# Performance work log

Measured on AMD Instinct MI355X. Metric: run time of the kernel, lower is better.

## Reference

```python
import jax, jax.numpy as jnp
import numpy as np

N_CLASSES = 19


def setup_inputs() -> dict:
    key = jax.random.key(0)
    k1, k2 = jax.random.split(key)
    embedding = jax.random.normal(k1, (4, 32, 128, 128), dtype=jnp.float32)
    label = jax.random.randint(k2, (4, 512, 512), 0, N_CLASSES, dtype=jnp.int64)
    return {"embedding": embedding, "label": label}


def _discriminative_loss(embedding, label, n_classes=N_CLASSES):
    N, H, W = label.shape
    C = embedding.shape[1]
    # bilinear upsample embedding to label resolution (F.upsample mode='bilinear')
    emb = jax.image.resize(embedding, (N, C, H, W), method="bilinear")
    HW = H * W
    emb = emb.reshape(N, C, HW).transpose(0, 2, 1)          # (N, HW, C)
    lab = label.reshape(N, HW)                               # (N, HW)

    onehot = jax.nn.one_hot(lab, n_classes, dtype=emb.dtype)  # (N, HW, K)
    count = onehot.sum(1)                                    # (N, K)
    mask = (count > 0).astype(emb.dtype)                     # (N, K)

    # per-class embedding sum and (biased, /(count+1)) mean
    cls_sum = jnp.einsum("npc,npk->nkc", emb, onehot)       # (N, K, C)
    cls_mean = cls_sum / (count[:, :, None] + 1.0)           # (N, K, C)

    # intra-class: per-pixel squared distance to own-class mean, mean over C
    mean_pp = jnp.take_along_axis(cls_mean, lab[:, :, None], axis=1)  # (N, HW, C)
    d2 = jnp.mean((emb - mean_pp) ** 2, axis=-1)             # (N, HW)
    intra_per_cls = jnp.einsum("np,npk->nk", d2, onehot) / (count + 1.0)  # (N, K)
    n_fg = mask[:, 1:].sum(1)                                # (N,)
    l2_intra = (intra_per_cls[:, 1:] * mask[:, 1:]).sum(1) / n_fg  # (N,)

    # inter-class: pairwise mean squared distance between class means
    diff = cls_mean[:, :, None, :] - cls_mean[:, None, :, :]  # (N, K, K, C)
    inter = jnp.mean(diff ** 2, axis=-1)                     # (N, K, K)
    inter = inter * mask[:, None, :] * mask[:, :, None]
    l2_inter = inter[:, 1:, 1:].reshape(N, -1).sum(1) / (n_fg * n_fg)  # (N,)

    return l2_intra - l2_inter


def reference(embedding, label):
    return _discriminative_loss(embedding, label)
```

## Files before the change

### kernel.cpp

```cpp
#include <hip/hip_runtime.h>

#define NIMG 4
#define NCLS 19
#define CCH  32
#define LH   128
#define LW   128
#define HH   512
#define WW   512
#define HWQ  (LH*LW)
#define HWP  (HH*WW)

#define TR 8
#define TC 16
#define NTX (LW/TC)
#define NTY (LH/TR)
#define NTILE (NTY*NTX)
#define TCELLS (TR*TC)
#define HALO_R (TR*4+4)
#define HALO_C (TC*4+4)

#define QB 64

__device__ __forceinline__ void taps(int v, int lim, int& i0, int& i1, float& f) {
    int r = v & 3;
    int b = (v >> 2) + ((r < 2) ? -1 : 0);
    f = 0.125f + 0.25f * (float)((r + 2) & 3);
    i0 = b < 0 ? 0 : b;
    i1 = (b + 1 > lim) ? lim : (b + 1);
}

__global__ __launch_bounds__(256) void k_field(const float* __restrict__ E,
        const int* __restrict__ lab, float* __restrict__ P_sum, float* __restrict__ P_cnt) {
    int tile = blockIdx.x, n = blockIdx.y;
    int ty = tile >> 3, tx = tile & 7;
    int Y0 = ty * TR, X0 = tx * TC;
    __shared__ float A[TCELLS * NCLS];
    __shared__ float red[8 * NCLS * CCH];
    int tid = threadIdx.x;
    for (int i = tid; i < TCELLS * NCLS; i += 256) A[i] = 0.f;
    __syncthreads();

    const int* ln = lab + (size_t)n * HWP;
    int h_lo = Y0 * 4 - 2, w_lo = X0 * 4 - 2;
    for (int i = tid; i < HALO_R * HALO_C; i += 256) {
        int hr = i / HALO_C, wc = i - hr * HALO_C;
        int h = h_lo + hr, w = w_lo + wc;
        if (h < 0 || h >= HH || w < 0 || w >= WW) continue;
        int L = ln[h * WW + w];
        int y0, y1, x0, x1; float fy, fx;
        taps(h, LH - 1, y0, y1, fy);
        taps(w, LW - 1, x0, x1, fx);
        int yy[2] = {y0, y1}; float wy[2] = {1.f - fy, fy};
        int xx[2] = {x0, x1}; float wx[2] = {1.f - fx, fx};
#pragma unroll
        for (int a = 0; a < 2; a++) {
#pragma unroll
            for (int b = 0; b < 2; b++) {
                int ry = yy[a] - Y0, rx = xx[b] - X0;
                if (ry >= 0 && ry < TR && rx >= 0 && rx < TC)
                    atomicAdd(&A[(ry * TC + rx) * NCLS + L], wy[a] * wx[b]);
            }
        }
    }
    __syncthreads();

    int g = tid >> 5, c = tid & 31;
    const float* Ec = E + ((size_t)n * CCH + c) * HWQ;
    float acc[NCLS];
#pragma unroll
    for (int k = 0; k < NCLS; k++) acc[k] = 0.f;
#pragma unroll
    for (int j = 0; j < TCELLS / 8; j++) {
        int cell = g * (TCELLS / 8) + j;
        int cy = cell >> 4, cx = cell & 15;
        float e = Ec[(Y0 + cy) * LW + (X0 + cx)];
        const float* Ar = &A[cell * NCLS];
#pragma unroll
        for (int k = 0; k < NCLS; k++) acc[k] = fmaf(Ar[k], e, acc[k]);
    }
#pragma unroll
    for (int k = 0; k < NCLS; k++) red[(g * NCLS + k) * CCH + c] = acc[k];
    __syncthreads();

    float* Ps = P_sum + (size_t)(n * NTILE + tile) * (NCLS * CCH);
    for (int idx = tid; idx < NCLS * CCH; idx += 256) {
        float s = 0.f;
#pragma unroll
        for (int gg = 0; gg < 8; gg++) s += red[gg * NCLS * CCH + idx];
        Ps[idx] = s;
    }
    if (tid < NCLS) {
        float s = 0.f;
        for (int cell = 0; cell < TCELLS; cell++) s += A[cell * NCLS + tid];
        P_cnt[(size_t)(n * NTILE + tile) * NCLS + tid] = s;
    }
}

__global__ __launch_bounds__(256) void k_quad(const float* __restrict__ E,
        const int* __restrict__ lab, float* __restrict__ P_S2) {
    int n = blockIdx.y;
    int q = blockIdx.x * 256 + threadIdx.x;
    int by = q >> 7, bx = q & 127;
    __shared__ float accS2[NCLS];
    if (threadIdx.x < NCLS) accS2[threadIdx.x] = 0.f;
    __syncthreads();

    const float* En = E + (size_t)n * CCH * HWQ;
    int r0 = (by == 0) ? 0 : by - 1;
    int r2 = (by == LH - 1) ? LH - 1 : by + 1;
    int c0 = (bx == 0) ? 0 : bx - 1;
    int c2 = (bx == LW - 1) ? LW - 1 : bx + 1;
    int o0 = r0 * LW, o1 = by * LW, o2 = r2 * LW;

    float d2[16];
#pragma unroll
    for (int i = 0; i < 16; i++) d2[i] = 0.f;

    for (int c = 0; c < CCH; c++) {
        const float* Ep = En + (size_t)c * HWQ;
        float e00 = Ep[o0 + c0], e01 = Ep[o0 + bx], e02 = Ep[o0 + c2];
        float e10 = Ep[o1 + c0], e11 = Ep[o1 + bx], e12 = Ep[o1 + c2];
        float e20 = Ep[o2 + c0], e21 = Ep[o2 + bx], e22 = Ep[o2 + c2];
        float dy0 = e10 - e00, dy1 = e11 - e01, dy2 = e12 - e02;
        float dz0 = e20 - e10, dz1 = e21 - e11, dz2 = e22 - e12;
        float ry[4][3];
        ry[0][0] = fmaf(0.625f, dy0, e00); ry[0][1] = fmaf(0.625f, dy1, e01); ry[0][2] = fmaf(0.625f, dy2, e02);
        ry[1][0] = fmaf(0.875f, dy0, e00); ry[1][1] = fmaf(0.875f, dy1, e01); ry[1][2] = fmaf(0.875f, dy2, e02);
        ry[2][0] = fmaf(0.125f, dz0, e10); ry[2][1] = fmaf(0.125f, dz1, e11); ry[2][2] = fmaf(0.125f, dz2, e12);
        ry[3][0] = fmaf(0.375f, dz0, e10); ry[3][1] = fmaf(0.375f, dz1, e11); ry[3][2] = fmaf(0.375f, dz2, e12);
#pragma unroll
        for (int r = 0; r < 4; r++) {
            float da = ry[r][1] - ry[r][0], db = ry[r][2] - ry[r][1];
            float v0 = fmaf(0.625f, da, ry[r][0]);
            float v1 = fmaf(0.875f, da, ry[r][0]);
            float v2 = fmaf(0.125f, db, ry[r][1]);
            float v3 = fmaf(0.375f, db, ry[r][1]);
            d2[r * 4 + 0] = fmaf(v0, v0, d2[r * 4 + 0]);
            d2[r * 4 + 1] = fmaf(v1, v1, d2[r * 4 + 1]);
            d2[r * 4 + 2] = fmaf(v2, v2, d2[r * 4 + 2]);
            d2[r * 4 + 3] = fmaf(v3, v3, d2[r * 4 + 3]);
        }
    }
    const int* lp = lab + (size_t)n * HWP + (by * 4) * WW + bx * 4;
#pragma unroll
    for (int r = 0; r < 4; r++) {
        int4 l4 = *(const int4*)(lp + r * WW);
        atomicAdd(&accS2[l4.x], d2[r * 4 + 0]);
        atomicAdd(&accS2[l4.y], d2[r * 4 + 1]);
        atomicAdd(&accS2[l4.z], d2[r * 4 + 2]);
        atomicAdd(&accS2[l4.w], d2[r * 4 + 3]);
    }
    __syncthreads();
    if (threadIdx.x < NCLS)
        P_S2[(size_t)(n * QB + blockIdx.x) * NCLS + threadIdx.x] = accS2[threadIdx.x];
}

__global__ __launch_bounds__(384) void k_final(const float* __restrict__ P_sum,
        const float* __restrict__ P_cnt, const float* __restrict__ P_S2,
        float* __restrict__ out) {
    int n = blockIdx.x, t = threadIdx.x;
    __shared__ float csum[NCLS * 33];
    __shared__ float m[NCLS * 33];
    __shared__ float cnt[NCLS];
    __shared__ float S2[NCLS];
    __shared__ float sIntra, sNfg, sInter;

    if (t == 0) sInter = 0.f;
    if (t < NCLS) {
        float s = 0.f;
        const float* p = P_cnt + (size_t)n * NTILE * NCLS + t;
        for (int b = 0; b < NTILE; b++) s += p[b * NCLS];
        cnt[t] = s;
        float s2 = 0.f;
        const float* p2 = P_S2 + (size_t)n * QB * NCLS + t;
        for (int b = 0; b < QB; b++) s2 += p2[b * NCLS];
        S2[t] = s2;
    }
    for (int idx = t; idx < NCLS * CCH; idx += 384) {
        float s = 0.f;
        const float* p = P_sum + (size_t)n * NTILE * NCLS * CCH + idx;
        for (int b = 0; b < NTILE; b++) s += p[b * NCLS * CCH];
        csum[(idx >> 5) * 33 + (idx & 31)] = s;
    }
    __syncthreads();
    for (int idx = t; idx < NCLS * CCH; idx += 384) {
        int k = idx >> 5, c = idx & 31;
        m[k * 33 + c] = csum[k * 33 + c] / (cnt[k] + 1.f);
    }
    __syncthreads();

    float vi = 0.f, fg = 0.f;
    if (t >= 1 && t < NCLS && cnt[t] > 0.f) {
        fg = 1.f;
        float dot = 0.f, mm = 0.f;
        for (int c = 0; c < CCH; c++) {
            float mv = m[t * 33 + c];
            dot = fmaf(mv, csum[t * 33 + c], dot);
            mm = fmaf(mv, mv, mm);
        }
        vi = (S2[t] - 2.f * dot + cnt[t] * mm) * (1.f / 32.f) / (cnt[t] + 1.f);
    }
#pragma unroll
    for (int s_ = 32; s_ >= 1; s_ >>= 1) { vi += __shfl_xor(vi, s_); fg += __shfl_xor(fg, s_); }
    if (t == 0) { sIntra = vi; sNfg = fg; }

    float ve = 0.f;
    if (t < 324) {
        int j = 1 + t / 18, k = 1 + t % 18;
        if (cnt[j] > 0.f && cnt[k] > 0.f) {
            float s = 0.f;
            for (int c = 0; c < CCH; c++) {
                float d = m[j * 33 + c] - m[k * 33 + c];
                s = fmaf(d, d, s);
            }
            ve = s * (1.f / 32.f);
        }
    }
#pragma unroll
    for (int s_ = 32; s_ >= 1; s_ >>= 1) ve += __shfl_xor(ve, s_);
    if ((t & 63) == 0) atomicAdd(&sInter, ve);
    __syncthreads();
    if (t == 0) out[n] = sIntra / sNfg - sInter / (sNfg * sNfg);
}

extern "C" void kernel_launch(void* const* d_in, const int* in_sizes, int n_in,
                              void* d_out, int out_size, void* d_ws, size_t ws_size,
                              hipStream_t stream) {
    const float* E = (const float*)d_in[0];
    const int* lab = (const int*)d_in[1];
    float* out = (float*)d_out;

    float* ws = (float*)d_ws;
    float* P_sum = ws;
    float* P_cnt = P_sum + (size_t)NIMG * NTILE * NCLS * CCH;
    float* P_S2  = P_cnt + (size_t)NIMG * NTILE * NCLS;

    k_field<<<dim3(NTILE, NIMG), dim3(256), 0, stream>>>(E, lab, P_sum, P_cnt);
    k_quad <<<dim3(QB, NIMG),    dim3(256), 0, stream>>>(E, lab, P_S2);
    k_final<<<dim3(NIMG),        dim3(384), 0, stream>>>(P_sum, P_cnt, P_S2, out);
}
```

Measured before the change: 119.6 us.

## Merge field and quad kernels into one launch with LDS-staged embedding tiles

The per-tile class-sum kernel and the per-pixel squared-norm kernel are fused into one launch whose blocks branch on blockIdx, removing a kernel launch and letting both workloads run concurrently. The field path now stages the embedding tile in padded LDS and reduces across half-waves with shuffles, cutting strided global reads. The quad path splits channels across two halves of each block, so it launches twice as many blocks over rows. The partial buffers are transposed so the final kernel can reduce counts and S2 with coalesced loads and wave shuffles. In exchange, the split quad path issues more label loads and LDS atomics, and blocks with different LDS and register needs share one kernel, which may limit occupancy.

Result: no change. 120.1 us (+0.4%).

```diff
diff --git a/kernel.cpp b/kernel.cpp
--- a/kernel.cpp
+++ b/kernel.cpp
@@ -12,14 +12,16 @@
 
 #define TR 8
 #define TC 16
-#define NTX (LW/TC)
-#define NTY (LH/TR)
-#define NTILE (NTY*NTX)
-#define TCELLS (TR*TC)
-#define HALO_R (TR*4+4)
-#define HALO_C (TC*4+4)
-
-#define QB 64
+#define NTILE 128
+#define TCELLS 128
+#define HALO_R 36
+#define HALO_C 68
+#define QROWS 128
+
+#define L_ET  0
+#define L_A   4224
+#define L_RED 6656
+#define LDS_FLOATS 9088
 
 __device__ __forceinline__ void taps(int v, int lim, int& i0, int& i1, float& f) {
     int r = v & 3;
@@ -29,162 +31,175 @@
     i1 = (b + 1 > lim) ? lim : (b + 1);
 }
 
-__global__ __launch_bounds__(256) void k_field(const float* __restrict__ E,
-        const int* __restrict__ lab, float* __restrict__ P_sum, float* __restrict__ P_cnt) {
-    int tile = blockIdx.x, n = blockIdx.y;
-    int ty = tile >> 3, tx = tile & 7;
-    int Y0 = ty * TR, X0 = tx * TC;
-    __shared__ float A[TCELLS * NCLS];
-    __shared__ float red[8 * NCLS * CCH];
-    int tid = threadIdx.x;
-    for (int i = tid; i < TCELLS * NCLS; i += 256) A[i] = 0.f;
-    __syncthreads();
-
-    const int* ln = lab + (size_t)n * HWP;
-    int h_lo = Y0 * 4 - 2, w_lo = X0 * 4 - 2;
-    for (int i = tid; i < HALO_R * HALO_C; i += 256) {
-        int hr = i / HALO_C, wc = i - hr * HALO_C;
-        int h = h_lo + hr, w = w_lo + wc;
-        if (h < 0 || h >= HH || w < 0 || w >= WW) continue;
-        int L = ln[h * WW + w];
-        int y0, y1, x0, x1; float fy, fx;
-        taps(h, LH - 1, y0, y1, fy);
-        taps(w, LW - 1, x0, x1, fx);
-        int yy[2] = {y0, y1}; float wy[2] = {1.f - fy, fy};
-        int xx[2] = {x0, x1}; float wx[2] = {1.f - fx, fx};
-#pragma unroll
-        for (int a = 0; a < 2; a++) {
-#pragma unroll
-            for (int b = 0; b < 2; b++) {
-                int ry = yy[a] - Y0, rx = xx[b] - X0;
-                if (ry >= 0 && ry < TR && rx >= 0 && rx < TC)
-                    atomicAdd(&A[(ry * TC + rx) * NCLS + L], wy[a] * wx[b]);
+__global__ __launch_bounds__(256) void k_main(const float* __restrict__ E,
+        const int* __restrict__ lab, float* __restrict__ P_sum,
+        float* __restrict__ P_cnt, float* __restrict__ P_S2) {
+    __shared__ float lds[LDS_FLOATS];
+    const int n = blockIdx.y;
+    const int tid = threadIdx.x;
+
+    if (blockIdx.x < NTILE) {
+        const int tile = blockIdx.x;
+        const int ty = tile >> 3, tx = tile & 7;
+        const int Y0 = ty * TR, X0 = tx * TC;
+
+        for (int i = tid; i < TCELLS * NCLS; i += 256) lds[L_A + i] = 0.f;
+#pragma unroll
+        for (int it = 0; it < 16; it++) {
+            int idx = it * 256 + tid;
+            int c = idx >> 7, cell = idx & 127;
+            int cy = cell >> 4, cx = cell & 15;
+            float e = E[((size_t)n * CCH + c) * HWQ + (Y0 + cy) * LW + (X0 + cx)];
+            lds[L_ET + cell * 33 + c] = e;
+        }
+        __syncthreads();
+
+        const int* ln = lab + (size_t)n * HWP;
+        int h_lo = Y0 * 4 - 2, w_lo = X0 * 4 - 2;
+        for (int i = tid; i < HALO_R * HALO_C; i += 256) {
+            int hr = i / HALO_C, wc = i - hr * HALO_C;
+            int h = h_lo + hr, w = w_lo + wc;
+            if (h < 0 || h >= HH || w < 0 || w >= WW) continue;
+            int L = ln[h * WW + w];
+            int y0, y1, x0, x1; float fy, fx;
+            taps(h, LH - 1, y0, y1, fy);
+            taps(w, LW - 1, x0, x1, fx);
+            int yy[2] = {y0, y1}; float wy[2] = {1.f - fy, fy};
+            int xx[2] = {x0, x1}; float wx[2] = {1.f - fx, fx};
+#pragma unroll
+            for (int a = 0; a < 2; a++) {
+#pragma unroll
+                for (int b = 0; b < 2; b++) {
+                    int ry = yy[a] - Y0, rx = xx[b] - X0;
+                    if (ry >= 0 && ry < TR && rx >= 0 && rx < TC)
+                        atomicAdd(&lds[L_A + (ry * TC + rx) * NCLS + L], wy[a] * wx[b]);
+                }
             }
         }
-    }
-    __syncthreads();
-
-    int g = tid >> 5, c = tid & 31;
-    const float* Ec = E + ((size_t)n * CCH + c) * HWQ;
-    float acc[NCLS];
-#pragma unroll
-    for (int k = 0; k < NCLS; k++) acc[k] = 0.f;
-#pragma unroll
-    for (int j = 0; j < TCELLS / 8; j++) {
-        int cell = g * (TCELLS / 8) + j;
-        int cy = cell >> 4, cx = cell & 15;
-        float e = Ec[(Y0 + cy) * LW + (X0 + cx)];
-        const float* Ar = &A[cell * NCLS];
-#pragma unroll
-        for (int k = 0; k < NCLS; k++) acc[k] = fmaf(Ar[k], e, acc[k]);
-    }
-#pragma unroll
-    for (int k = 0; k < NCLS; k++) red[(g * NCLS + k) * CCH + c] = acc[k];
-    __syncthreads();
-
-    float* Ps = P_sum + (size_t)(n * NTILE + tile) * (NCLS * CCH);
-    for (int idx = tid; idx < NCLS * CCH; idx += 256) {
-        float s = 0.f;
-#pragma unroll
-        for (int gg = 0; gg < 8; gg++) s += red[gg * NCLS * CCH + idx];
-        Ps[idx] = s;
-    }
-    if (tid < NCLS) {
-        float s = 0.f;
-        for (int cell = 0; cell < TCELLS; cell++) s += A[cell * NCLS + tid];
-        P_cnt[(size_t)(n * NTILE + tile) * NCLS + tid] = s;
-    }
-}
-
-__global__ __launch_bounds__(256) void k_quad(const float* __restrict__ E,
-        const int* __restrict__ lab, float* __restrict__ P_S2) {
-    int n = blockIdx.y;
-    int q = blockIdx.x * 256 + threadIdx.x;
-    int by = q >> 7, bx = q & 127;
-    __shared__ float accS2[NCLS];
-    if (threadIdx.x < NCLS) accS2[threadIdx.x] = 0.f;
-    __syncthreads();
-
-    const float* En = E + (size_t)n * CCH * HWQ;
-    int r0 = (by == 0) ? 0 : by - 1;
-    int r2 = (by == LH - 1) ? LH - 1 : by + 1;
-    int c0 = (bx == 0) ? 0 : bx - 1;
-    int c2 = (bx == LW - 1) ? LW - 1 : bx + 1;
-    int o0 = r0 * LW, o1 = by * LW, o2 = r2 * LW;
-
-    float d2[16];
-#pragma unroll
-    for (int i = 0; i < 16; i++) d2[i] = 0.f;
-
-    for (int c = 0; c < CCH; c++) {
-        const float* Ep = En + (size_t)c * HWQ;
-        float e00 = Ep[o0 + c0], e01 = Ep[o0 + bx], e02 = Ep[o0 + c2];
-        float e10 = Ep[o1 + c0], e11 = Ep[o1 + bx], e12 = Ep[o1 + c2];
-        float e20 = Ep[o2 + c0], e21 = Ep[o2 + bx], e22 = Ep[o2 + c2];
-        float dy0 = e10 - e00, dy1 = e11 - e01, dy2 = e12 - e02;
-        float dz0 = e20 - e10, dz1 = e21 - e11, dz2 = e22 - e12;
-        float ry[4][3];
-        ry[0][0] = fmaf(0.625f, dy0, e00); ry[0][1] = fmaf(0.625f, dy1, e01); ry[0][2] = fmaf(0.625f, dy2, e02);
-        ry[1][0] = fmaf(0.875f, dy0, e00); ry[1][1] = fmaf(0.875f, dy1, e01); ry[1][2] = fmaf(0.875f, dy2, e02);
-        ry[2][0] = fmaf(0.125f, dz0, e10); ry[2][1] = fmaf(0.125f, dz1, e11); ry[2][2] = fmaf(0.125f, dz2, e12);
-        ry[3][0] = fmaf(0.375f, dz0, e10); ry[3][1] = fmaf(0.375f, dz1, e11); ry[3][2] = fmaf(0.375f, dz2, e12);
+        __syncthreads();
+
+        const int g = tid >> 5, c = tid & 31;
+        float acc[NCLS];
+#pragma unroll
+        for (int k = 0; k < NCLS; k++) acc[k] = 0.f;
+#pragma unroll
+        for (int j = 0; j < 16; j++) {
+            int cell = g * 16 + j;
+            float e = lds[L_ET + cell * 33 + c];
+            const float* Ar = &lds[L_A + cell * NCLS];
+#pragma unroll
+            for (int k = 0; k < NCLS; k++) acc[k] = fmaf(Ar[k], e, acc[k]);
+        }
+#pragma unroll
+        for (int k = 0; k < NCLS; k++) acc[k] += __shfl_xor(acc[k], 32);
+        const int wave = tid >> 6;
+        if ((tid & 63) < 32) {
+#pragma unroll
+            for (int k = 0; k < NCLS; k++)
+                lds[L_RED + wave * 608 + k * 32 + c] = acc[k];
+        }
+        __syncthreads();
+
+        float* Ps = P_sum + (size_t)(n * NTILE + tile) * (NCLS * CCH);
+        for (int i = tid; i < NCLS * CCH; i += 256) {
+            float s = lds[L_RED + i] + lds[L_RED + 608 + i]
+                    + lds[L_RED + 1216 + i] + lds[L_RED + 1824 + i];
+            Ps[i] = s;
+        }
+        if (tid < NCLS) {
+            float s = 0.f;
+            for (int cell = 0; cell < TCELLS; cell++) s += lds[L_A + cell * NCLS + tid];
+            P_cnt[((size_t)n * NCLS + tid) * NTILE + tile] = s;
+        }
+    } else {
+        const int by = blockIdx.x - NTILE;
+        const int half = tid >> 7, bx = tid & 127;
+        if (tid < NCLS) lds[tid] = 0.f;
+        __syncthreads();
+
+        const float* En = E + ((size_t)n * CCH + half * 16) * HWQ;
+        int r0 = (by == 0) ? 0 : by - 1;
+        int r2 = (by == LH - 1) ? LH - 1 : by + 1;
+        int c0 = (bx == 0) ? 0 : bx - 1;
+        int c2 = (bx == LW - 1) ? LW - 1 : bx + 1;
+        int o0 = r0 * LW, o1 = by * LW, o2 = r2 * LW;
+
+        float d2[16];
+#pragma unroll
+        for (int i = 0; i < 16; i++) d2[i] = 0.f;
+
+#pragma unroll
+        for (int c = 0; c < 16; c++) {
+            const float* Ep = En + (size_t)c * HWQ;
+            float e00 = Ep[o0 + c0], e01 = Ep[o0 + bx], e02 = Ep[o0 + c2];
+            float e10 = Ep[o1 + c0], e11 = Ep[o1 + bx], e12 = Ep[o1 + c2];
+            float e20 = Ep[o2 + c0], e21 = Ep[o2 + bx], e22 = Ep[o2 + c2];
+            float dy0 = e10 - e00, dy1 = e11 - e01, dy2 = e12 - e02;
+            float dz0 = e20 - e10, dz1 = e21 - e11, dz2 = e22 - e12;
+            float ry[4][3];
+            ry[0][0] = fmaf(0.625f, dy0, e00); ry[0][1] = fmaf(0.625f, dy1, e01); ry[0][2] = fmaf(0.625f, dy2, e02);
+            ry[1][0] = fmaf(0.875f, dy0, e00); ry[1][1] = fmaf(0.875f, dy1, e01); ry[1][2] = fmaf(0.875f, dy2, e02);
+            ry[2][0] = fmaf(0.125f, dz0, e10); ry[2][1] = fmaf(0.125f, dz1, e11); ry[2][2] = fmaf(0.125f, dz2, e12);
+            ry[3][0] = fmaf(0.375f, dz0, e10); ry[3][1] = fmaf(0.375f, dz1, e11); ry[3][2] = fmaf(0.375f, dz2, e12);
+#pragma unroll
+            for (int r = 0; r < 4; r++) {
+                float da = ry[r][1] - ry[r][0], db = ry[r][2] - ry[r][1];
+                float v0 = fmaf(0.625f, da, ry[r][0]);
+                float v1 = fmaf(0.875f, da, ry[r][0]);
+                float v2 = fmaf(0.125f, db, ry[r][1]);
+                float v3 = fmaf(0.375f, db, ry[r][1]);
+                d2[r * 4 + 0] = fmaf(v0, v0, d2[r * 4 + 0]);
+                d2[r * 4 + 1] = fmaf(v1, v1, d2[r * 4 + 1]);
+                d2[r * 4 + 2] = fmaf(v2, v2, d2[r * 4 + 2]);
+                d2[r * 4 + 3] = fmaf(v3, v3, d2[r * 4 + 3]);
+            }
+        }
+        const int* lp = lab + (size_t)n * HWP + (by * 4) * WW + bx * 4;
 #pragma unroll
         for (int r = 0; r < 4; r++) {
-            float da = ry[r][1] - ry[r][0], db = ry[r][2] - ry[r][1];
-            float v0 = fmaf(0.625f, da, ry[r][0]);
-            float v1 = fmaf(0.875f, da, ry[r][0]);
-            float v2 = fmaf(0.125f, db, ry[r][1]);
-            float v3 = fmaf(0.375f, db, ry[r][1]);
-            d2[r * 4 + 0] = fmaf(v0, v0, d2[r * 4 + 0]);
-            d2[r * 4 + 1] = fmaf(v1, v1, d2[r * 4 + 1]);
-            d2[r * 4 + 2] = fmaf(v2, v2, d2[r * 4 + 2]);
-            d2[r * 4 + 3] = fmaf(v3, v3, d2[r * 4 + 3]);
-        }
-    }
-    const int* lp = lab + (size_t)n * HWP + (by * 4) * WW + bx * 4;
-#pragma unroll
-    for (int r = 0; r < 4; r++) {
-        int4 l4 = *(const int4*)(lp + r * WW);
-        atomicAdd(&accS2[l4.x], d2[r * 4 + 0]);
-        atomicAdd(&accS2[l4.y], d2[r * 4 + 1]);
-        atomicAdd(&accS2[l4.z], d2[r * 4 + 2]);
-        atomicAdd(&accS2[l4.w], d2[r * 4 + 3]);
-    }
-    __syncthreads();
-    if (threadIdx.x < NCLS)
-        P_S2[(size_t)(n * QB + blockIdx.x) * NCLS + threadIdx.x] = accS2[threadIdx.x];
-}
-
-__global__ __launch_bounds__(384) void k_final(const float* __restrict__ P_sum,
+            int4 l4 = *(const int4*)(lp + r * WW);
+            atomicAdd(&lds[l4.x], d2[r * 4 + 0]);
+            atomicAdd(&lds[l4.y], d2[r * 4 + 1]);
+            atomicAdd(&lds[l4.z], d2[r * 4 + 2]);
+            atomicAdd(&lds[l4.w], d2[r * 4 + 3]);
+        }
+        __syncthreads();
+        if (tid < NCLS)
+            P_S2[((size_t)n * NCLS + tid) * QROWS + by] = lds[tid];
+    }
+}
+
+__global__ __launch_bounds__(640) void k_final(const float* __restrict__ P_sum,
         const float* __restrict__ P_cnt, const float* __restrict__ P_S2,
         float* __restrict__ out) {
-    int n = blockIdx.x, t = threadIdx.x;
+    const int n = blockIdx.x, t = threadIdx.x;
     __shared__ float csum[NCLS * 33];
     __shared__ float m[NCLS * 33];
     __shared__ float cnt[NCLS];
     __shared__ float S2[NCLS];
     __shared__ float sIntra, sNfg, sInter;
-
     if (t == 0) sInter = 0.f;
-    if (t < NCLS) {
+
+    if (t < NCLS * CCH) {
+        const int k = t >> 5, c = t & 31;
+        const float* p = P_sum + (size_t)n * NTILE * (NCLS * CCH) + t;
         float s = 0.f;
-        const float* p = P_cnt + (size_t)n * NTILE * NCLS + t;
-        for (int b = 0; b < NTILE; b++) s += p[b * NCLS];
-        cnt[t] = s;
-        float s2 = 0.f;
-        const float* p2 = P_S2 + (size_t)n * QB * NCLS + t;
-        for (int b = 0; b < QB; b++) s2 += p2[b * NCLS];
-        S2[t] = s2;
-    }
-    for (int idx = t; idx < NCLS * CCH; idx += 384) {
-        float s = 0.f;
-        const float* p = P_sum + (size_t)n * NTILE * NCLS * CCH + idx;
-        for (int b = 0; b < NTILE; b++) s += p[b * NCLS * CCH];
-        csum[(idx >> 5) * 33 + (idx & 31)] = s;
+        for (int b = 0; b < NTILE; b++) s += p[b * (NCLS * CCH)];
+        csum[k * 33 + c] = s;
+        const float* pc = P_cnt + ((size_t)n * NCLS + k) * NTILE;
+        float sc = pc[c] + pc[c + 32] + pc[c + 64] + pc[c + 96];
+        const float* ps = P_S2 + ((size_t)n * NCLS + k) * QROWS;
+        float s2 = ps[c] + ps[c + 32] + ps[c + 64] + ps[c + 96];
+#pragma unroll
+        for (int mk = 16; mk >= 1; mk >>= 1) {
+            sc += __shfl_xor(sc, mk);
+            s2 += __shfl_xor(s2, mk);
+        }
+        if (c == 0) { cnt[k] = sc; S2[k] = s2; }
     }
     __syncthreads();
-    for (int idx = t; idx < NCLS * CCH; idx += 384) {
-        int k = idx >> 5, c = idx & 31;
+    if (t < NCLS * CCH) {
+        const int k = t >> 5, c = t & 31;
         m[k * 33 + c] = csum[k * 33 + c] / (cnt[k] + 1.f);
     }
     __syncthreads();
@@ -193,6 +208,7 @@
     if (t >= 1 && t < NCLS && cnt[t] > 0.f) {
         fg = 1.f;
         float dot = 0.f, mm = 0.f;
+#pragma unroll
         for (int c = 0; c < CCH; c++) {
             float mv = m[t * 33 + c];
             dot = fmaf(mv, csum[t * 33 + c], dot);
@@ -209,6 +225,7 @@
         int j = 1 + t / 18, k = 1 + t % 18;
         if (cnt[j] > 0.f && cnt[k] > 0.f) {
             float s = 0.f;
+#pragma unroll
             for (int c = 0; c < CCH; c++) {
                 float d = m[j * 33 + c] - m[k * 33 + c];
                 s = fmaf(d, d, s);
@@ -233,9 +250,8 @@
     float* ws = (float*)d_ws;
     float* P_sum = ws;
     float* P_cnt = P_sum + (size_t)NIMG * NTILE * NCLS * CCH;
-    float* P_S2  = P_cnt + (size_t)NIMG * NTILE * NCLS;
-
-    k_field<<<dim3(NTILE, NIMG), dim3(256), 0, stream>>>(E, lab, P_sum, P_cnt);
-    k_quad <<<dim3(QB, NIMG),    dim3(256), 0, stream>>>(E, lab, P_S2);
-    k_final<<<dim3(NIMG),        dim3(384), 0, stream>>>(P_sum, P_cnt, P_S2, out);
-}
+    float* P_S2  = P_cnt + (size_t)NIMG * NCLS * NTILE;
+
+    k_main <<<dim3(NTILE + QROWS, NIMG), dim3(256), 0, stream>>>(E, lab, P_sum, P_cnt, P_S2);
+    k_final<<<dim3(NIMG), dim3(640), 0, stream>>>(P_sum, P_cnt, P_S2, out);
+}
```
